# Kernel tuning notes

Hardware: AMD Instinct MI355X
Metric: run time of the kernel (lower is better)

The kernel has to match this reference:

```python
import jax, jax.numpy as jnp
import numpy as np

# ---- module constants (from init_kwargs) ----
N_POLES = 80          # N -> dictionary width 2N+1 = 161
T_SEQ = 36            # T
LAM_F = 0.1           # lam_f
RMIN, RMAX = 0.8, 1.1 # r_r
TMIN, TMAX = 0.1, np.pi  # r_t
NSAMPLE, DDATA = 128, 50
MAX_ITER = 100


def real_D(T, rho, theta):
    # CONSTR=True path: clamp poles into the valid annulus/sector
    rho = jnp.clip(rho, RMIN, RMAX)
    theta = jnp.clip(theta, TMIN, TMAX)
    i = jnp.arange(T, dtype=rho.dtype)[:, None]            # [T,1]
    p = jnp.power(rho[None, :], i)                          # [T,N] rho^i
    W1 = p * jnp.cos(i * theta[None, :])                    # [T,N]
    W2 = p * jnp.sin(i * theta[None, :])                    # [T,N]
    ones = jnp.ones((T, 1), dtype=rho.dtype)
    return jnp.concatenate([ones, W1, W2], axis=1)          # [T, 2N+1]


def fista_reweighted(D, Y, lambd, w, max_iter=MAX_ITER):
    # D: [T,Np], Y: [n,T,d], w: [n,Np,d]
    Np = D.shape[1]
    DtD = D.T @ D                                           # [Np,Np]
    DtY = jnp.einsum('tp,ntd->npd', D, Y)                   # [n,Np,d]
    L = jnp.linalg.norm(DtD, ord=2)                         # spectral norm
    Linv = 1.0 / L
    wl = w * (lambd * Linv)
    A = jnp.eye(Np, dtype=D.dtype) - DtD * Linv             # [Np,Np]
    c_minus = DtY * Linv - wl
    c_plus = DtY * Linv + wl
    x0 = jnp.zeros_like(DtY)

    def step(carry, _):
        x, y, t, done = carry
        Ay = jnp.einsum('pq,nqd->npd', A, y)
        # soft-threshold via max/min split (as in source)
        x_new = jnp.maximum(Ay + c_minus, 0.0) + jnp.minimum(Ay + c_plus, 0.0)
        t_new = (1.0 + jnp.sqrt(1.0 + 4.0 * t * t)) / 2.0
        tt = (t - 1.0) / t_new
        y_new = x_new + tt * (x_new - x)
        conv = jnp.linalg.norm(x - x_new) / Np < 1e-5       # global check
        x_o = jnp.where(done, x, x_new)
        y_o = jnp.where(done, y, y_new)
        t_o = jnp.where(done, t, t_new)
        return (x_o, y_o, t_o, done | conv), None

    step = jax.checkpoint(step)
    init = (x0, x0, jnp.asarray(1.0, D.dtype), jnp.asarray(False))
    (x, _, _, _), _ = jax.lax.scan(step, init, None, length=max_iter)
    return x


def rh_fista(D, Y, lam):
    Np = D.shape[1]
    w = jnp.ones((Y.shape[0], Np, Y.shape[2]), dtype=Y.dtype)
    C = None
    for _ in range(2):  # fixed 2 reweighting rounds, as in source
        C = fista_reweighted(D, Y, lam, w)
        w_raw = 1.0 / (jnp.abs(C) + 0.01)
        w = w_raw / jnp.sum(jnp.abs(w_raw), axis=1, keepdims=True) * Np
    R = jnp.einsum('tp,npd->ntd', D, C)
    return C, D, R


def setup_inputs() -> dict:
    key = jax.random.key(0)
    k1, k2, k3 = jax.random.split(key, 3)
    x = jax.random.normal(k1, (NSAMPLE, T_SEQ, DDATA), dtype=jnp.float32)
    rho = jax.random.uniform(k2, (N_POLES,), dtype=jnp.float32) * (RMAX - RMIN) + RMIN
    theta = jax.random.uniform(k3, (N_POLES,), dtype=jnp.float32) * (TMAX - TMIN) + TMIN
    return {"x": x, "rho": rho, "theta": theta}


def reference(x, rho, theta):
    D = real_D(T_SEQ, rho, theta)            # [T, 2N+1]
    C, D, R = rh_fista(D, x, LAM_F)          # wiRH=True path
    return C, D, R
```

## Files before the change

### kernel.cpp

```cpp
#include <hip/hip_runtime.h>
#include <math.h>

#define NPOLES 80
#define NP 161
#define NPAD 164
#define TSEQ 36
#define NSAMP 128
#define DDATA 50
#define LAMF 0.1f
#define NPD (NP*DDATA)
#define TD (TSEQ*DDATA)
#define CSIZE (NSAMP*NPD)
#define RSIZE (NSAMP*TD)
#define DSIZE (TSEQ*NP)

#define RT_N 11
#define KC_N 5
#define FRAG_CHUNK 512
#define YK 168

typedef __attribute__((ext_vector_type(8))) short s8b;
typedef __attribute__((ext_vector_type(4))) float f4;

__device__ __forceinline__ unsigned short f2b(float f) {
    unsigned u = __float_as_uint(f);
    unsigned r = (u + 0x7FFFu + ((u >> 16) & 1u)) >> 16;
    return (unsigned short)r;
}
__device__ __forceinline__ float b2f(unsigned short h) {
    return __uint_as_float(((unsigned)h) << 16);
}

__global__ void k_build_D(const float* __restrict__ rho, const float* __restrict__ theta,
                          float* __restrict__ Dw, float* __restrict__ Dout) {
    int idx = blockIdx.x * 256 + threadIdx.x;
    if (idx >= DSIZE) return;
    int t = idx / NP, p = idx - (idx / NP) * NP;
    float v;
    if (p == 0) {
        v = 1.f;
    } else {
        int j = (p <= NPOLES) ? (p - 1) : (p - 1 - NPOLES);
        float r  = fminf(fmaxf(rho[j],   0.8f), 1.1f);
        float th = fminf(fmaxf(theta[j], 0.1f), 3.14159265358979323846f);
        double pw  = pow((double)r, (double)t);
        double ang = (double)t * (double)th;
        v = (float)(pw * ((p <= NPOLES) ? cos(ang) : sin(ang)));
    }
    Dw[idx] = v;
    Dout[idx] = v;
}

__global__ void k_ddt(const float* __restrict__ Dw, float* __restrict__ DDt) {
    int idx = blockIdx.x * 256 + threadIdx.x;
    if (idx >= TSEQ * TSEQ) return;
    int i = idx / TSEQ, j = idx - (idx / TSEQ) * TSEQ;
    float acc = 0.f;
    for (int p = 0; p < NP; ++p) acc = fmaf(Dw[i * NP + p], Dw[j * NP + p], acc);
    DDt[idx] = acc;
}

__global__ void k_power(const float* __restrict__ DDt, float* __restrict__ scal) {
    __shared__ float sM[TSEQ * TSEQ];
    __shared__ float sv[TSEQ];
    int tid = threadIdx.x;
    for (int i = tid; i < TSEQ * TSEQ; i += 64) sM[i] = DDt[i];
    if (tid < TSEQ) sv[tid] = 1.f;
    __syncthreads();
    for (int it = 0; it < 150; ++it) {
        float u = 0.f;
        if (tid < TSEQ) {
            for (int q = 0; q < TSEQ; ++q) u = fmaf(sM[tid * TSEQ + q], sv[q], u);
        }
        float nn = u * u;
        for (int o = 32; o > 0; o >>= 1) nn += __shfl_down(nn, o);
        nn = __shfl(nn, 0);
        float inv = rsqrtf(nn);
        __syncthreads();
        if (tid < TSEQ) sv[tid] = u * inv;
        __syncthreads();
    }
    float rq = 0.f;
    if (tid < TSEQ) {
        float uu = 0.f;
        for (int q = 0; q < TSEQ; ++q) uu = fmaf(sM[tid * TSEQ + q], sv[q], uu);
        rq = uu * sv[tid];
    }
    for (int o = 32; o > 0; o >>= 1) rq += __shfl_down(rq, o);
    if (tid == 0) { scal[0] = 1.f / rq; scal[1] = rq; }
}

__global__ void k_A(const float* __restrict__ Dw, const float* __restrict__ scal,
                    float* __restrict__ Apad) {
    int idx = blockIdx.x * 256 + threadIdx.x;
    if (idx >= NP * NPAD) return;
    int q = idx / NPAD, p = idx - (idx / NPAD) * NPAD;
    float v = 0.f;
    if (p < NP) {
        float acc = 0.f;
        for (int t = 0; t < TSEQ; ++t) acc = fmaf(Dw[t * NP + q], Dw[t * NP + p], acc);
        v = ((p == q) ? 1.f : 0.f) - acc * scal[0];
    }
    Apad[idx] = v;
}

__global__ void k_dty(const float* __restrict__ Dw, const float* __restrict__ Y,
                      float* __restrict__ dty) {
    int idx = blockIdx.x * 256 + threadIdx.x;
    if (idx >= CSIZE) return;
    int n = idx / NPD;
    int r = idx - n * NPD;
    int p = r / DDATA;
    int d = r - p * DDATA;
    const float* yp = Y + n * TD + d;
    float acc = 0.f;
    for (int t = 0; t < TSEQ; ++t) acc = fmaf(Dw[t * NP + p], yp[t * DDATA], acc);
    dty[idx] = acc;
}

__global__ void k_Afrag(const float* __restrict__ Apad,
                        short* __restrict__ AfH, short* __restrict__ AfL) {
    int idx = blockIdx.x * 256 + threadIdx.x;
    if (idx >= RT_N * KC_N * 64) return;
    int lane = idx & 63;
    int chunk = idx >> 6;
    int kc = chunk % KC_N;
    int rt = chunk / KC_N;
    int p = rt * 16 + (lane & 15);
    int q0 = kc * 32 + (lane >> 4) * 8;
    int base = chunk * FRAG_CHUNK + lane * 8;
#pragma unroll
    for (int j = 0; j < 8; ++j) {
        int q = q0 + j;
        float v = (p < NP && q < NP) ? Apad[q * NPAD + p] : 0.f;
        unsigned short h = f2b(v);
        float rem = v - b2f(h);
        AfH[base + j] = (short)h;
        AfL[base + j] = (short)f2b(rem);
    }
}

__global__ __launch_bounds__(256, 2) void k_fista(
    const float* __restrict__ Apad,
    const s8b* __restrict__ AfH, const s8b* __restrict__ AfL,
    const float* __restrict__ dty_g, const float* __restrict__ scal,
    float* __restrict__ Cout)
{
    __shared__ unsigned short Yh[16][YK];
    __shared__ unsigned short Yl[16][YK];
    __shared__ float yrem[16];
    __shared__ float colpart[4][16];
    __shared__ float sS[16];

    const int tid = threadIdx.x;
    const int n  = blockIdx.x >> 2;
    const int dq = blockIdx.x & 3;
    const int w = tid >> 6;
    const int lane = tid & 63;
    const int c0 = lane & 15;
    const int g = lane >> 4;
    const int rt0 = w * 3;
    const int ntr = (w == 3) ? 2 : 3;
    const int ncol = (dq == 3) ? 11 : 13;
    const int colv = dq * 13 + c0;
    const bool cvalid = c0 < ncol;
    const float Linv = scal[0];
    const float lamL = LAMF * Linv;

    s8b ahr[3][KC_N], alr[3][KC_N];
    const s8b zer = {0, 0, 0, 0, 0, 0, 0, 0};
#pragma unroll
    for (int rr = 0; rr < 3; ++rr) {
#pragma unroll
        for (int kc = 0; kc < KC_N; ++kc) {
            if (rr < ntr) {
                int ck = (rt0 + rr) * KC_N + kc;
                ahr[rr][kc] = AfH[ck * 64 + lane];
                alr[rr][kc] = AfL[ck * 64 + lane];
            } else {
                ahr[rr][kc] = zer;
                alr[rr][kc] = zer;
            }
        }
    }

    int rowb[3];
    float dtL[3][4];
    f4 a160r[3];
#pragma unroll
    for (int rr = 0; rr < 3; ++rr) {
        rowb[rr] = (rt0 + rr) * 16 + g * 4;
#pragma unroll
        for (int r = 0; r < 4; ++r) {
            int row = rowb[rr] + r;
            float v = 0.f;
            if ((rr < ntr) && row < NP && cvalid)
                v = dty_g[n * NPD + row * DDATA + colv];
            dtL[rr][r] = v * Linv;
            a160r[rr][r] = ((rr < ntr) && row < NP) ? Apad[160 * NPAD + row] : 0.f;
        }
    }

    float x_[3][4], wlam_[3][4];
#pragma unroll
    for (int rr = 0; rr < 3; ++rr)
#pragma unroll
        for (int r = 0; r < 4; ++r) wlam_[rr][r] = lamL;

#pragma unroll 1
    for (int round = 0; round < 2; ++round) {
#pragma unroll
        for (int rr = 0; rr < 3; ++rr)
#pragma unroll
            for (int r = 0; r < 4; ++r) x_[rr][r] = 0.f;
        {
            unsigned* ph = (unsigned*)&Yh[0][0];
            unsigned* pl = (unsigned*)&Yl[0][0];
            for (int i = tid; i < 16 * YK / 2; i += 256) { ph[i] = 0u; pl[i] = 0u; }
            if (tid < 16) yrem[tid] = 0.f;
        }
        float tmom = 1.f;
        __syncthreads();

#pragma unroll 1
        for (int it = 0; it < 100; ++it) {
            float tn = (1.f + sqrtf(fmaf(4.f * tmom, tmom, 1.f))) * 0.5f;
            float ttc = (tmom - 1.f) / tn;
            tmom = tn;

            f4 acc[3];
#pragma unroll
            for (int rr = 0; rr < 3; ++rr) acc[rr] = (f4){0.f, 0.f, 0.f, 0.f};

#pragma unroll
            for (int kc = 0; kc < KC_N; ++kc) {
                int yo = kc * 32 + g * 8;
                s8b bh = *(const s8b*)&Yh[c0][yo];
                s8b bl = *(const s8b*)&Yl[c0][yo];
#pragma unroll
                for (int rr = 0; rr < 3; ++rr) {
                    if (rr < ntr) {
                        acc[rr] = __builtin_amdgcn_mfma_f32_16x16x32_bf16(ahr[rr][kc], bh, acc[rr], 0, 0, 0);
                        acc[rr] = __builtin_amdgcn_mfma_f32_16x16x32_bf16(ahr[rr][kc], bl, acc[rr], 0, 0, 0);
                        acc[rr] = __builtin_amdgcn_mfma_f32_16x16x32_bf16(alr[rr][kc], bh, acc[rr], 0, 0, 0);
                    }
                }
            }
            {
                float yv = yrem[c0];
#pragma unroll
                for (int rr = 0; rr < 3; ++rr)
                    if (rr < ntr) acc[rr] += a160r[rr] * yv;
            }
            __syncthreads();

#pragma unroll
            for (int rr = 0; rr < 3; ++rr) {
                if (rr < ntr) {
                    unsigned short hh[4], ll[4];
                    float yn0 = 0.f;
#pragma unroll
                    for (int r = 0; r < 4; ++r) {
                        float bb = dtL[rr][r] + acc[rr][r];
                        float wl = wlam_[rr][r];
                        float xn = fmaxf(bb - wl, 0.f) + fminf(bb + wl, 0.f);
                        float yn = fmaf(ttc, xn - x_[rr][r], xn);
                        x_[rr][r] = xn;
                        if (r == 0) yn0 = yn;
                        unsigned short h = f2b(yn);
                        hh[r] = h;
                        ll[r] = f2b(yn - b2f(h));
                    }
                    int rt = rt0 + rr;
                    if (rt < 10) {
                        uint2 hp, lp;
                        hp.x = (unsigned)hh[0] | ((unsigned)hh[1] << 16);
                        hp.y = (unsigned)hh[2] | ((unsigned)hh[3] << 16);
                        lp.x = (unsigned)ll[0] | ((unsigned)ll[1] << 16);
                        lp.y = (unsigned)ll[2] | ((unsigned)ll[3] << 16);
                        *(uint2*)&Yh[c0][rowb[rr]] = hp;
                        *(uint2*)&Yl[c0][rowb[rr]] = lp;
                    } else if (g == 0) {
                        yrem[c0] = yn0;
                    }
                }
            }
            __syncthreads();
        }

        if (round == 0) {
            float ps = 0.f;
#pragma unroll
            for (int rr = 0; rr < 3; ++rr) {
                if (rr < ntr) {
#pragma unroll
                    for (int r = 0; r < 4; ++r) {
                        if (rowb[rr] + r < NP)
                            ps += 1.f / (fabsf(x_[rr][r]) + 0.01f);
                    }
                }
            }
            ps += __shfl_xor(ps, 16);
            ps += __shfl_xor(ps, 32);
            if (lane < 16) colpart[w][lane] = ps;
            __syncthreads();
            if (tid < 16) {
                float s = colpart[0][tid] + colpart[1][tid] + colpart[2][tid] + colpart[3][tid];
                sS[tid] = (float)NP / s;
            }
            __syncthreads();
            float sc = sS[c0] * lamL;
#pragma unroll
            for (int rr = 0; rr < 3; ++rr)
#pragma unroll
                for (int r = 0; r < 4; ++r)
                    wlam_[rr][r] = (1.f / (fabsf(x_[rr][r]) + 0.01f)) * sc;
            __syncthreads();
        }
    }

#pragma unroll
    for (int rr = 0; rr < 3; ++rr) {
        if ((rr < ntr) && cvalid) {
#pragma unroll
            for (int r = 0; r < 4; ++r) {
                int row = rowb[rr] + r;
                if (row < NP)
                    Cout[n * NPD + row * DDATA + colv] = x_[rr][r];
            }
        }
    }
}

__global__ void k_R(const float* __restrict__ Dw, const float* __restrict__ Cf,
                    float* __restrict__ Rout) {
    int idx = blockIdx.x * 256 + threadIdx.x;
    if (idx >= RSIZE) return;
    int n = idx / TD;
    int r = idx - n * TD;
    int t = r / DDATA;
    int d = r - t * DDATA;
    const float* xp = Cf + n * NPD + d;
    float acc = 0.f;
    for (int p = 0; p < NP; ++p) acc = fmaf(Dw[t * NP + p], xp[p * DDATA], acc);
    Rout[idx] = acc;
}

extern "C" void kernel_launch(void* const* d_in, const int* in_sizes, int n_in,
                              void* d_out, int out_size, void* d_ws, size_t ws_size,
                              hipStream_t stream) {
    const float* Y     = (const float*)d_in[0];
    const float* rho   = (const float*)d_in[1];
    const float* theta = (const float*)d_in[2];
    float* Cout = (float*)d_out;
    float* Dout = Cout + CSIZE;
    float* Rout = Dout + DSIZE;

    float* ws    = (float*)d_ws;
    float* Dw    = ws;
    float* Apad  = Dw + 5824;
    float* DDt   = Apad + 26416;
    float* scal  = DDt + 1312;
    float* dty   = scal + 16;
    float* AfH_f = dty + CSIZE;
    float* AfL_f = AfH_f + 14080;

    k_build_D<<<(DSIZE + 255) / 256, 256, 0, stream>>>(rho, theta, Dw, Dout);
    k_ddt<<<(TSEQ * TSEQ + 255) / 256, 256, 0, stream>>>(Dw, DDt);
    k_power<<<1, 64, 0, stream>>>(DDt, scal);
    k_A<<<(NP * NPAD + 255) / 256, 256, 0, stream>>>(Dw, scal, Apad);
    k_dty<<<(CSIZE + 255) / 256, 256, 0, stream>>>(Dw, Y, dty);
    k_Afrag<<<(RT_N * KC_N * 64 + 255) / 256, 256, 0, stream>>>(Apad, (short*)AfH_f, (short*)AfL_f);

    k_fista<<<NSAMP * 4, 256, 0, stream>>>(Apad, (const s8b*)AfH_f, (const s8b*)AfL_f,
                                           dty, scal, Cout);

    k_R<<<(RSIZE + 255) / 256, 256, 0, stream>>>(Dw, Cout, Rout);
}
```

Baseline: 430.4 us.

## Double-buffer Y in LDS to drop one barrier per FISTA iteration

Gives the bf16 hi/lo Y tiles and the remainder row in shared memory two buffers. Each iteration reads from the current buffer and writes to the next, which removes the barrier between the MFMA reads and the writes. The change also seeds the accumulators with DtY/L, writes soft-thresholding as a clamp, and replaces round-to-nearest bf16 conversion with truncation packed via perm. Truncation changes the hi/lo split but keeps the sum exact in principle. The cost is double the LDS footprint for Y, which may affect occupancy.

```diff
diff --git a/kernel.cpp b/kernel.cpp
--- a/kernel.cpp
+++ b/kernel.cpp
@@ -146,9 +146,9 @@
     const float* __restrict__ dty_g, const float* __restrict__ scal,
     float* __restrict__ Cout)
 {
-    __shared__ unsigned short Yh[16][YK];
-    __shared__ unsigned short Yl[16][YK];
-    __shared__ float yrem[16];
+    __shared__ unsigned short Yh[2][16][YK];
+    __shared__ unsigned short Yl[2][16][YK];
+    __shared__ float yrem[2][16];
     __shared__ float colpart[4][16];
     __shared__ float sS[16];
 
@@ -214,12 +214,13 @@
 #pragma unroll
             for (int r = 0; r < 4; ++r) x_[rr][r] = 0.f;
         {
-            unsigned* ph = (unsigned*)&Yh[0][0];
-            unsigned* pl = (unsigned*)&Yl[0][0];
+            unsigned* ph = (unsigned*)&Yh[0][0][0];
+            unsigned* pl = (unsigned*)&Yl[0][0][0];
             for (int i = tid; i < 16 * YK / 2; i += 256) { ph[i] = 0u; pl[i] = 0u; }
-            if (tid < 16) yrem[tid] = 0.f;
+            if (tid < 16) yrem[0][tid] = 0.f;
         }
         float tmom = 1.f;
+        int cur = 0;
         __syncthreads();
 
 #pragma unroll 1
@@ -227,16 +228,19 @@
             float tn = (1.f + sqrtf(fmaf(4.f * tmom, tmom, 1.f))) * 0.5f;
             float ttc = (tmom - 1.f) / tn;
             tmom = tn;
+            const int nxt = cur ^ 1;
 
             f4 acc[3];
 #pragma unroll
-            for (int rr = 0; rr < 3; ++rr) acc[rr] = (f4){0.f, 0.f, 0.f, 0.f};
+            for (int rr = 0; rr < 3; ++rr)
+#pragma unroll
+                for (int r = 0; r < 4; ++r) acc[rr][r] = dtL[rr][r];
 
 #pragma unroll
             for (int kc = 0; kc < KC_N; ++kc) {
                 int yo = kc * 32 + g * 8;
-                s8b bh = *(const s8b*)&Yh[c0][yo];
-                s8b bl = *(const s8b*)&Yl[c0][yo];
+                s8b bh = *(const s8b*)&Yh[cur][c0][yo];
+                s8b bl = *(const s8b*)&Yl[cur][c0][yo];
 #pragma unroll
                 for (int rr = 0; rr < 3; ++rr) {
                     if (rr < ntr) {
@@ -247,45 +251,49 @@
                 }
             }
             {
-                float yv = yrem[c0];
+                float yv = yrem[cur][c0];
 #pragma unroll
                 for (int rr = 0; rr < 3; ++rr)
-                    if (rr < ntr) acc[rr] += a160r[rr] * yv;
-            }
-            __syncthreads();
+                    if (rr < ntr)
+#pragma unroll
+                        for (int r = 0; r < 4; ++r)
+                            acc[rr][r] = fmaf(a160r[rr][r], yv, acc[rr][r]);
+            }
 
 #pragma unroll
             for (int rr = 0; rr < 3; ++rr) {
                 if (rr < ntr) {
-                    unsigned short hh[4], ll[4];
+                    unsigned yb[4], rb[4];
                     float yn0 = 0.f;
 #pragma unroll
                     for (int r = 0; r < 4; ++r) {
-                        float bb = dtL[rr][r] + acc[rr][r];
+                        float bb = acc[rr][r];
                         float wl = wlam_[rr][r];
-                        float xn = fmaxf(bb - wl, 0.f) + fminf(bb + wl, 0.f);
+                        float cl = fminf(fmaxf(bb, -wl), wl);
+                        float xn = bb - cl;
                         float yn = fmaf(ttc, xn - x_[rr][r], xn);
                         x_[rr][r] = xn;
                         if (r == 0) yn0 = yn;
-                        unsigned short h = f2b(yn);
-                        hh[r] = h;
-                        ll[r] = f2b(yn - b2f(h));
+                        unsigned u = __float_as_uint(yn);
+                        yb[r] = u;
+                        rb[r] = __float_as_uint(yn - __uint_as_float(u & 0xFFFF0000u));
                     }
                     int rt = rt0 + rr;
                     if (rt < 10) {
                         uint2 hp, lp;
-                        hp.x = (unsigned)hh[0] | ((unsigned)hh[1] << 16);
-                        hp.y = (unsigned)hh[2] | ((unsigned)hh[3] << 16);
-                        lp.x = (unsigned)ll[0] | ((unsigned)ll[1] << 16);
-                        lp.y = (unsigned)ll[2] | ((unsigned)ll[3] << 16);
-                        *(uint2*)&Yh[c0][rowb[rr]] = hp;
-                        *(uint2*)&Yl[c0][rowb[rr]] = lp;
+                        hp.x = __builtin_amdgcn_perm(yb[1], yb[0], 0x07060302u);
+                        hp.y = __builtin_amdgcn_perm(yb[3], yb[2], 0x07060302u);
+                        lp.x = __builtin_amdgcn_perm(rb[1], rb[0], 0x07060302u);
+                        lp.y = __builtin_amdgcn_perm(rb[3], rb[2], 0x07060302u);
+                        *(uint2*)&Yh[nxt][c0][rowb[rr]] = hp;
+                        *(uint2*)&Yl[nxt][c0][rowb[rr]] = lp;
                     } else if (g == 0) {
-                        yrem[c0] = yn0;
+                        yrem[nxt][c0] = yn0;
                     }
                 }
             }
             __syncthreads();
+            cur = nxt;
         }
 
         if (round == 0) {
```

Result: faster. 394.8 us (-8.3%).
